# Performance work log

Measured on AMD Instinct MI355X. Metric: run time of the kernel, lower is better.

The kernel has to match this reference:

```python
import jax, jax.numpy as jnp
import numpy as np

E, T, D, H = 32, 65536, 512, 1024


def setup_inputs() -> dict:
    key = jax.random.key(0)
    k = jax.random.split(key, 7)
    norm = lambda kk, shp, sc: (jax.random.normal(kk, shp, jnp.float32) * sc)
    x = norm(k[0], (T, D), 1.0)
    w1 = norm(k[1], (E, D, H), D ** -0.5)   # per-expert up-proj (gate branch)
    b1 = norm(k[2], (E, H), 0.02)
    w3 = norm(k[3], (E, D, H), D ** -0.5)   # per-expert up-proj (linear branch)
    b3 = norm(k[4], (E, H), 0.02)
    w2 = norm(k[5], (E, H, D), H ** -0.5)   # per-expert down-proj
    b2 = norm(k[6], (E, D), 0.02)
    # tokens are pre-sorted by expert; uniform dispatch of T//E tokens per expert
    group_sizes = jnp.full((E,), T // E, jnp.int32)
    return dict(x=x, w1=w1, b1=b1, w3=w3, b3=b3, w2=w2, b2=b2,
                group_sizes=group_sizes)


def reference(x, w1, b1, w3, b3, w2, b2, group_sizes):
    # expert id per token, derived from contiguous group sizes
    bounds = jnp.cumsum(group_sizes)                       # [E]
    seg = jnp.searchsorted(bounds, jnp.arange(x.shape[0]), side='right')  # [T]
    # grouped GEMMs: per-expert weight bank applied to its contiguous token slab
    h1 = jax.lax.ragged_dot(x, w1, group_sizes) + b1[seg]  # [T,H]
    h3 = jax.lax.ragged_dot(x, w3, group_sizes) + b3[seg]  # [T,H]
    h = jax.nn.silu(h1) * h3                               # SwiGLU gate
    out = jax.lax.ragged_dot(h, w2, group_sizes) + b2[seg] # [T,D]
    return out
```

## Files before the change

### kernel.cpp

```cpp
#include <hip/hip_runtime.h>
#include <hip/hip_bf16.h>

#define TOK 65536
#define NE  32
#define DD  512
#define HH  1024
#define TPE 2048

typedef short s16x8  __attribute__((ext_vector_type(8)));
typedef float f32x16 __attribute__((ext_vector_type(16)));
using u16 = unsigned short;
using u32 = unsigned int;

__device__ __forceinline__ u16 f2bf(float f) {
  __bf16 h = (__bf16)f;
  return __builtin_bit_cast(u16, h);
}
__device__ __forceinline__ u32 pk2(float lo, float hi) {
  return (u32)f2bf(lo) | ((u32)f2bf(hi) << 16);
}
__device__ __forceinline__ int swz(int row, int colb) {
  return (row << 7) + (colb ^ ((row & 7) << 4));
}

#define MFMA(a, b, c) __builtin_amdgcn_mfma_f32_32x32x16_bf16(a, b, c, 0, 0, 0)
#define GLD(src, dst) __builtin_amdgcn_global_load_lds( \
    (const __attribute__((address_space(1))) void*)(src), \
    (__attribute__((address_space(3))) void*)(dst), 16, 0, 0)
#define SETP(n) __builtin_amdgcn_s_setprio(n)
#define SCHEDB() __builtin_amdgcn_sched_barrier(0)
#define SBAR()  __builtin_amdgcn_s_barrier()

__global__ __launch_bounds__(256) void p1_cvt_x(
    const float* __restrict__ x, u16* __restrict__ xb) {
  const size_t i = ((size_t)blockIdx.x * 256 + threadIdx.x) * 8;
  const float4 a = *(const float4*)(x + i);
  const float4 b = *(const float4*)(x + i + 4);
  uint4 v;
  v.x = pk2(a.x, a.y); v.y = pk2(a.z, a.w);
  v.z = pk2(b.x, b.y); v.w = pk2(b.z, b.w);
  *(uint4*)(xb + i) = v;
}

__global__ __launch_bounds__(256) void p2_w13t(
    const float* __restrict__ w1, const float* __restrict__ w3,
    u16* __restrict__ w13t) {
  __shared__ __align__(16) u16 L1[64 * 72], L3[64 * 72];
  const int bid = blockIdx.x;
  const int e = bid >> 7, rr = bid & 127;
  const int d0 = (rr & 7) << 6, h0 = (rr >> 3) << 6;
  const int t = threadIdx.x;
  const float* const s1 = w1 + (size_t)e * DD * HH + (size_t)d0 * HH + h0;
  const float* const s3 = w3 + (size_t)e * DD * HH + (size_t)d0 * HH + h0;
  const int cg = (t & 15) << 2, rbase = t >> 4;
#pragma unroll
  for (int j = 0; j < 4; ++j) {
    const int dr = rbase + (j << 4);
    const float4 a = *(const float4*)(s1 + (size_t)dr * HH + cg);
    const float4 b = *(const float4*)(s3 + (size_t)dr * HH + cg);
    L1[(cg + 0) * 72 + dr] = f2bf(a.x); L1[(cg + 1) * 72 + dr] = f2bf(a.y);
    L1[(cg + 2) * 72 + dr] = f2bf(a.z); L1[(cg + 3) * 72 + dr] = f2bf(a.w);
    L3[(cg + 0) * 72 + dr] = f2bf(b.x); L3[(cg + 1) * 72 + dr] = f2bf(b.y);
    L3[(cg + 2) * 72 + dr] = f2bf(b.z); L3[(cg + 3) * 72 + dr] = f2bf(b.w);
  }
  __syncthreads();
  u16* const dst = w13t + (size_t)e * (2 * HH) * DD;
  const int cb8 = (t & 7) << 3;
#pragma unroll
  for (int j = 0; j < 2; ++j) {
    const int nloc = (t >> 3) + (j << 5);
    const int n = h0 + nloc;
    const int R1 = ((n >> 5) << 6) + (n & 31);
    const uint4 v1 = *(const uint4*)(L1 + nloc * 72 + cb8);
    const uint4 v3 = *(const uint4*)(L3 + nloc * 72 + cb8);
    *(uint4*)(dst + (size_t)R1 * DD + d0 + cb8) = v1;
    *(uint4*)(dst + (size_t)(R1 + 32) * DD + d0 + cb8) = v3;
  }
}

__global__ __launch_bounds__(256) void p3_w2t(
    const float* __restrict__ w2, u16* __restrict__ w2t) {
  __shared__ __align__(16) u16 L[64 * 72];
  const int bid = blockIdx.x;
  const int e = bid >> 7, rr = bid & 127;
  const int d0 = (rr & 7) << 6, h0 = (rr >> 3) << 6;
  const int t = threadIdx.x;
  const float* const s = w2 + (size_t)e * HH * DD + (size_t)h0 * DD + d0;
  const int cg = (t & 15) << 2, rbase = t >> 4;
#pragma unroll
  for (int j = 0; j < 4; ++j) {
    const int hr = rbase + (j << 4);
    const float4 a = *(const float4*)(s + (size_t)hr * DD + cg);
    L[(cg + 0) * 72 + hr] = f2bf(a.x); L[(cg + 1) * 72 + hr] = f2bf(a.y);
    L[(cg + 2) * 72 + hr] = f2bf(a.z); L[(cg + 3) * 72 + hr] = f2bf(a.w);
  }
  __syncthreads();
  u16* const dst = w2t + (size_t)e * DD * HH;
  const int cb8 = (t & 7) << 3;
#pragma unroll
  for (int j = 0; j < 2; ++j) {
    const int dloc = (t >> 3) + (j << 5);
    const uint4 v = *(const uint4*)(L + dloc * 72 + cb8);
    *(uint4*)(dst + (size_t)(d0 + dloc) * HH + h0 + cb8) = v;
  }
}

template <int MODE>
__global__ __launch_bounds__(512, 2) void gemm4s(
    const u16* __restrict__ A, const u16* __restrict__ Bm,
    const float* __restrict__ bx, const float* __restrict__ by,
    void* __restrict__ outp) {
  constexpr int K  = MODE ? HH : DD;
  constexpr int NT = K >> 6;
  constexpr int NB = MODE ? 2 : 8;
  constexpr int NWG = NE * 8 * NB;
  __shared__ __align__(16) char lds[131072];

  int bid = blockIdx.x;
  bid = (bid & 7) * (NWG / 8) + (bid >> 3);
  const int e   = bid / (8 * NB);
  const int rr  = bid % (8 * NB);
  const int m_t = rr & 7;
  const int n_t = rr >> 3;
  const int rowbase = e * TPE + (m_t << 8);

  const int t = threadIdx.x;
  const int wv = t >> 6, lane = t & 63;
  const int l31 = lane & 31, half = lane >> 5;
  const int wm = wv >> 2, wn = wv & 3;

  const u16* const Abase = A + (size_t)rowbase * K;
  const u16* const Bbase = Bm + ((size_t)e * NB + n_t) * 256 * K;

  int srcoff0, srcoff1;
  {
    const int c0 = t,       lr0 = c0 >> 3, s0 = (c0 & 7) ^ (lr0 & 7);
    const int c1 = 512 + t, lr1 = c1 >> 3, s1 = (c1 & 7) ^ (lr1 & 7);
    srcoff0 = ((lr0 << 1) | (s0 >> 2)) * K + ((s0 & 3) << 3);
    srcoff1 = ((lr1 << 1) | (s1 >> 2)) * K + ((s1 & 3) << 3);
  }
  const int t16 = t << 4;

  auto stageQ = [&](int tau, int q) {
    const u16* const src = ((q & 1) ? Bbase : Abase) + tau * 64 + (q >> 1) * 32;
    char* const dst = lds + ((tau & 1) << 16) + (q << 14);
    GLD(src + srcoff0, dst + t16);
    GLD(src + srcoff1, dst + 8192 + t16);
  };

  const int lrow_off = l31 >> 1;
  const int pbit = l31 & 1;
  const int sw7 = lrow_off & 7;
  const int sA0 = (((pbit << 2) | 0 | half) ^ sw7) << 4;
  const int sA1 = (((pbit << 2) | 2 | half) ^ sw7) << 4;
  const int aoff = ((wm << 6) + lrow_off) << 7;
  const int boff = ((wn << 5) + lrow_off) << 7;

  f32x16 acc[4][2] = {};
  s16x8 b00{}, b01{}, b10{}, b11{};

#define VM4 asm volatile("s_waitcnt vmcnt(4)" ::: "memory")
#define VM0 asm volatile("s_waitcnt vmcnt(0)" ::: "memory")
#define LGKM0 asm volatile("s_waitcnt lgkmcnt(0)" ::: "memory")
#define NOPV ((void)0)

#define PHASE(CB, KH, MH, DOB, STG, VM) do { \
  const char* const Aq = (CB) + ((KH) << 15); \
  const char* const Bq = Aq + 16384; \
  if (DOB) { \
    b00 = *(const s16x8*)(Bq + boff + 0 * 2048 + sA0); \
    b01 = *(const s16x8*)(Bq + boff + 1 * 2048 + sA0); \
    b10 = *(const s16x8*)(Bq + boff + 0 * 2048 + sA1); \
    b11 = *(const s16x8*)(Bq + boff + 1 * 2048 + sA1); \
  } \
  const s16x8 a0 = *(const s16x8*)(Aq + aoff + (2 * (MH)) * 2048 + sA0); \
  const s16x8 a1 = *(const s16x8*)(Aq + aoff + (2 * (MH)) * 2048 + sA1); \
  const s16x8 a2 = *(const s16x8*)(Aq + aoff + (2 * (MH) + 1) * 2048 + sA0); \
  const s16x8 a3 = *(const s16x8*)(Aq + aoff + (2 * (MH) + 1) * 2048 + sA1); \
  STG; VM; \
  SCHEDB(); SBAR(); LGKM0; SCHEDB(); \
  SETP(1); \
  acc[2 * (MH)][0]     = MFMA(a0, b00, acc[2 * (MH)][0]); \
  acc[2 * (MH)][1]     = MFMA(a0, b01, acc[2 * (MH)][1]); \
  acc[2 * (MH)][0]     = MFMA(a1, b10, acc[2 * (MH)][0]); \
  acc[2 * (MH)][1]     = MFMA(a1, b11, acc[2 * (MH)][1]); \
  acc[2 * (MH) + 1][0] = MFMA(a2, b00, acc[2 * (MH) + 1][0]); \
  acc[2 * (MH) + 1][1] = MFMA(a2, b01, acc[2 * (MH) + 1][1]); \
  acc[2 * (MH) + 1][0] = MFMA(a3, b10, acc[2 * (MH) + 1][0]); \
  acc[2 * (MH) + 1][1] = MFMA(a3, b11, acc[2 * (MH) + 1][1]); \
  SETP(0); \
} while (0)

  stageQ(0, 0); stageQ(0, 1); stageQ(0, 2); stageQ(0, 3);
  VM4; SCHEDB(); SBAR();

  for (int kt = 0; kt < NT - 1; ++kt) {
    const char* const cb = lds + ((kt & 1) << 16);
    PHASE(cb, 0, 0, true,  (stageQ(kt + 1, 0), stageQ(kt + 1, 1)), NOPV);
    PHASE(cb, 0, 1, false, NOPV, VM4);
    PHASE(cb, 1, 0, true,  (stageQ(kt + 1, 2), stageQ(kt + 1, 3)), NOPV);
    PHASE(cb, 1, 1, false, NOPV, VM4);
  }
  {
    const char* const cb = lds + (((NT - 1) & 1) << 16);
    PHASE(cb, 0, 0, true,  NOPV, NOPV);
    PHASE(cb, 0, 1, false, NOPV, VM0);
    PHASE(cb, 1, 0, true,  NOPV, NOPV);
    PHASE(cb, 1, 1, false, NOPV, NOPV);
  }

#undef PHASE
#undef VM4
#undef VM0
#undef LGKM0
#undef NOPV

  if constexpr (MODE == 0) {
    const int g = (n_t << 2) + wn;
    const int hcol = (g << 5) + l31;
    const float bv1 = bx[e * HH + hcol];
    const float bv3 = by[e * HH + hcol];
    u16* const hp = (u16*)outp;
#pragma unroll
    for (int mf = 0; mf < 4; ++mf) {
#pragma unroll
      for (int rg = 0; rg < 16; ++rg) {
        const int grow = rowbase + (wm << 7) + (mf << 5) +
                         (rg & 3) + ((rg >> 2) << 3) + (half << 2);
        const float s1 = acc[mf][0][rg] + bv1;
        const float s3 = acc[mf][1][rg] + bv3;
        hp[(size_t)grow * HH + hcol] = f2bf(s1 * s3 / (1.0f + __expf(-s1)));
      }
    }
  } else {
    float* const op = (float*)outp;
#pragma unroll
    for (int mf = 0; mf < 4; ++mf) {
#pragma unroll
      for (int nf = 0; nf < 2; ++nf) {
        const int col = (n_t << 8) + (wn << 6) + (nf << 5) + l31;
        const float bv = bx[e * DD + col];
#pragma unroll
        for (int rg = 0; rg < 16; ++rg) {
          const int grow = rowbase + (wm << 7) + (mf << 5) +
                           (rg & 3) + ((rg >> 2) << 3) + (half << 2);
          op[(size_t)grow * DD + col] = acc[mf][nf][rg] + bv;
        }
      }
    }
  }
}

__global__ __launch_bounds__(256, 2) void k1_up_swiglu(
    const float* __restrict__ x,  const float* __restrict__ w1,
    const float* __restrict__ b1, const float* __restrict__ w3,
    const float* __restrict__ b3, u16* __restrict__ hbuf) {
  __shared__ __align__(16) char lds[32768];
  char* const As  = lds;
  char* const B1s = lds + 16384;
  char* const B3s = lds + 24576;
  const int bid = blockIdx.x;
  const int e = bid >> 8, rr = bid & 255;
  const int m_t = rr & 15, n_t = rr >> 4;
  const int rowbase = e * TPE + (m_t << 7), colbase = n_t << 6;
  const int t = threadIdx.x, wv = t >> 6, lane = t & 63;
  const int l31 = lane & 31, half = lane >> 5;
  const int wm = wv >> 1, wn = wv & 1;
  const int ag = t & 15, am0 = t >> 4, bn = t & 63, bk0 = t >> 6;
  const float* const xb = x + (size_t)rowbase * DD + (ag << 2);
  const size_t woff = (size_t)e * (DD * HH) + colbase + bn;
  const float* const w1b = w1 + woff;
  const float* const w3b = w3 + woff;
  float4 ra[8]; float rb1[16], rb3[16];
  auto gload = [&](int kt) {
    const float* xp = xb + (kt << 6);
#pragma unroll
    for (int j = 0; j < 8; ++j)
      ra[j] = *(const float4*)(xp + (size_t)(am0 + (j << 4)) * DD);
#pragma unroll
    for (int j = 0; j < 2; ++j) {
      const int k0 = (kt << 6) + ((bk0 + (j << 2)) << 3);
#pragma unroll
      for (int i = 0; i < 8; ++i) {
        rb1[(j << 3) + i] = w1b[(size_t)(k0 + i) * HH];
        rb3[(j << 3) + i] = w3b[(size_t)(k0 + i) * HH];
      }
    }
  };
  f32x16 acc10 = {}, acc11 = {}, acc30 = {}, acc31 = {};
  gload(0);
  for (int kt = 0; kt < 8; ++kt) {
    if (kt) __syncthreads();
#pragma unroll
    for (int j = 0; j < 8; ++j) {
      const int m = am0 + (j << 4);
      uint2 v; v.x = pk2(ra[j].x, ra[j].y); v.y = pk2(ra[j].z, ra[j].w);
      *(uint2*)(As + swz(m, ag << 3)) = v;
    }
#pragma unroll
    for (int j = 0; j < 2; ++j) {
      const int kg = bk0 + (j << 2);
      uint4 v;
      v.x = pk2(rb1[(j << 3) + 0], rb1[(j << 3) + 1]);
      v.y = pk2(rb1[(j << 3) + 2], rb1[(j << 3) + 3]);
      v.z = pk2(rb1[(j << 3) + 4], rb1[(j << 3) + 5]);
      v.w = pk2(rb1[(j << 3) + 6], rb1[(j << 3) + 7]);
      *(uint4*)(B1s + swz(bn, kg << 4)) = v;
      v.x = pk2(rb3[(j << 3) + 0], rb3[(j << 3) + 1]);
      v.y = pk2(rb3[(j << 3) + 2], rb3[(j << 3) + 3]);
      v.z = pk2(rb3[(j << 3) + 4], rb3[(j << 3) + 5]);
      v.w = pk2(rb3[(j << 3) + 6], rb3[(j << 3) + 7]);
      *(uint4*)(B3s + swz(bn, kg << 4)) = v;
    }
    __syncthreads();
    if (kt < 7) gload(kt + 1);
#pragma unroll
    for (int kk = 0; kk < 4; ++kk) {
      const int colb = (kk << 5) + (half << 4);
      const s16x8 a0 = *(const s16x8*)(As  + swz((wm << 6) + l31,      colb));
      const s16x8 a1 = *(const s16x8*)(As  + swz((wm << 6) + 32 + l31, colb));
      const s16x8 f1 = *(const s16x8*)(B1s + swz((wn << 5) + l31,      colb));
      const s16x8 f3 = *(const s16x8*)(B3s + swz((wn << 5) + l31,      colb));
      acc10 = MFMA(a0, f1, acc10); acc30 = MFMA(a0, f3, acc30);
      acc11 = MFMA(a1, f1, acc11); acc31 = MFMA(a1, f3, acc31);
    }
  }
  const int gcol = colbase + (wn << 5) + l31;
  const float bv1 = b1[e * HH + gcol], bv3 = b3[e * HH + gcol];
  u16* const hp = hbuf + gcol;
#pragma unroll
  for (int mb = 0; mb < 2; ++mb) {
    const f32x16 A1 = mb ? acc11 : acc10;
    const f32x16 A3 = mb ? acc31 : acc30;
#pragma unroll
    for (int rg = 0; rg < 16; ++rg) {
      const int grow = rowbase + (wm << 6) + (mb << 5) +
                       (rg & 3) + ((rg >> 2) << 3) + (half << 2);
      const float s1 = A1[rg] + bv1, s3 = A3[rg] + bv3;
      hp[(size_t)grow * HH] = f2bf(s1 * s3 / (1.0f + __expf(-s1)));
    }
  }
}

__global__ __launch_bounds__(256, 2) void k2_down(
    const u16* __restrict__ hbuf, const float* __restrict__ w2,
    const float* __restrict__ b2, float* __restrict__ out) {
  __shared__ __align__(16) char lds[32768];
  char* const As = lds;
  char* const Bs = lds + 16384;
  const int bid = blockIdx.x;
  const int e = bid >> 6, rr = bid & 63;
  const int m_t = rr & 15, n_t = rr >> 4;
  const int rowbase = e * TPE + (m_t << 7), colbase = n_t << 7;
  const int t = threadIdx.x, wv = t >> 6, lane = t & 63;
  const int l31 = lane & 31, half = lane >> 5;
  const int wm = wv >> 1, wn = wv & 1;
  const int ag = t & 7, am0 = t >> 3, bnn = t & 127, bk0 = t >> 7;
  const u16* const hb = hbuf + (size_t)rowbase * HH + (ag << 3);
  const float* const w2b = w2 + (size_t)e * (HH * DD) + colbase + bnn;
  uint4 ra[4]; float rb[32];
  auto gload = [&](int kt) {
#pragma unroll
    for (int j = 0; j < 4; ++j)
      ra[j] = *(const uint4*)(hb + (size_t)(am0 + (j << 5)) * HH + (kt << 6));
#pragma unroll
    for (int j = 0; j < 4; ++j) {
      const int k0 = (kt << 6) + ((bk0 + (j << 1)) << 3);
#pragma unroll
      for (int i = 0; i < 8; ++i)
        rb[(j << 3) + i] = w2b[(size_t)(k0 + i) * DD];
    }
  };
  f32x16 c00 = {}, c01 = {}, c10 = {}, c11 = {};
  gload(0);
  for (int kt = 0; kt < 16; ++kt) {
    if (kt) __syncthreads();
#pragma unroll
    for (int j = 0; j < 4; ++j)
      *(uint4*)(As + swz(am0 + (j << 5), ag << 4)) = ra[j];
#pragma unroll
    for (int j = 0; j < 4; ++j) {
      const int kg = bk0 + (j << 1);
      uint4 v;
      v.x = pk2(rb[(j << 3) + 0], rb[(j << 3) + 1]);
      v.y = pk2(rb[(j << 3) + 2], rb[(j << 3) + 3]);
      v.z = pk2(rb[(j << 3) + 4], rb[(j << 3) + 5]);
      v.w = pk2(rb[(j << 3) + 6], rb[(j << 3) + 7]);
      *(uint4*)(Bs + swz(bnn, kg << 4)) = v;
    }
    __syncthreads();
    if (kt < 15) gload(kt + 1);
#pragma unroll
    for (int kk = 0; kk < 4; ++kk) {
      const int colb = (kk << 5) + (half << 4);
      const s16x8 af0 = *(const s16x8*)(As + swz((wm << 6) + l31,      colb));
      const s16x8 af1 = *(const s16x8*)(As + swz((wm << 6) + 32 + l31, colb));
      const s16x8 bf0 = *(const s16x8*)(Bs + swz((wn << 6) + l31,      colb));
      const s16x8 bf1 = *(const s16x8*)(Bs + swz((wn << 6) + 32 + l31, colb));
      c00 = MFMA(af0, bf0, c00); c01 = MFMA(af0, bf1, c01);
      c10 = MFMA(af1, bf0, c10); c11 = MFMA(af1, bf1, c11);
    }
  }
#pragma unroll
  for (int mb = 0; mb < 2; ++mb) {
#pragma unroll
    for (int nb = 0; nb < 2; ++nb) {
      const f32x16 c = mb ? (nb ? c11 : c10) : (nb ? c01 : c00);
      const int gcol = colbase + (wn << 6) + (nb << 5) + l31;
      const float bv = b2[e * DD + gcol];
#pragma unroll
      for (int rg = 0; rg < 16; ++rg) {
        const int grow = rowbase + (wm << 6) + (mb << 5) +
                         (rg & 3) + ((rg >> 2) << 3) + (half << 2);
        out[(size_t)grow * DD + gcol] = c[rg] + bv;
      }
    }
  }
}

extern "C" void kernel_launch(void* const* d_in, const int* in_sizes, int n_in,
                              void* d_out, int out_size, void* d_ws, size_t ws_size,
                              hipStream_t stream) {
  const float* x  = (const float*)d_in[0];
  const float* w1 = (const float*)d_in[1];
  const float* b1 = (const float*)d_in[2];
  const float* w3 = (const float*)d_in[3];
  const float* b3 = (const float*)d_in[4];
  const float* w2 = (const float*)d_in[5];
  const float* b2 = (const float*)d_in[6];

  const size_t W13T_B = (size_t)NE * 2 * HH * DD * 2;
  const size_t W2T_B  = (size_t)NE * DD * HH * 2;
  const size_t H_B    = (size_t)TOK * HH * 2;

  if (ws_size >= W13T_B + W2T_B + H_B) {
    u16* const xb   = (u16*)d_out;
    u16* const w13t = (u16*)d_ws;
    u16* const w2t  = (u16*)((char*)d_ws + W13T_B);
    u16* const hbuf = (u16*)((char*)d_ws + W13T_B + W2T_B);

    p1_cvt_x<<<dim3(TOK * DD / 2048), dim3(256), 0, stream>>>(x, xb);
    p2_w13t <<<dim3(NE * 128),        dim3(256), 0, stream>>>(w1, w3, w13t);
    p3_w2t  <<<dim3(NE * 128),        dim3(256), 0, stream>>>(w2, w2t);
    gemm4s<0><<<dim3(NE * 64), dim3(512), 0, stream>>>(xb, w13t, b1, b3, hbuf);
    gemm4s<1><<<dim3(NE * 16), dim3(512), 0, stream>>>(hbuf, w2t, b2, nullptr, d_out);
  } else {
    u16* hbuf = (ws_size >= H_B) ? (u16*)d_ws : (u16*)d_out;
    k1_up_swiglu<<<dim3(NE * 256), dim3(256), 0, stream>>>(x, w1, b1, w3, b3, hbuf);
    k2_down<<<dim3(NE * 64), dim3(256), 0, stream>>>(hbuf, w2, b2, (float*)d_out);
  }
}
```

Before: 366.3 us.

## Replace up-projection mega-tile GEMM with smaller single-buffered 128x128 tile kernel

```diff
diff --git a/kernel.cpp b/kernel.cpp
--- a/kernel.cpp
+++ b/kernel.cpp
@@ -105,14 +105,91 @@
   }
 }
 
-template <int MODE>
-__global__ __launch_bounds__(512, 2) void gemm4s(
+__global__ __launch_bounds__(256, 3) void g0_up(
     const u16* __restrict__ A, const u16* __restrict__ Bm,
     const float* __restrict__ bx, const float* __restrict__ by,
-    void* __restrict__ outp) {
-  constexpr int K  = MODE ? HH : DD;
+    u16* __restrict__ hp) {
+  constexpr int K = DD;
+  __shared__ __align__(16) char lds[32768];
+  char* const As = lds;
+  char* const Bs = lds + 16384;
+
+  int bid = blockIdx.x;
+  bid = (bid & 7) * (NE * 256 / 8) + (bid >> 3);
+  const int e   = bid >> 8;
+  const int rr  = bid & 255;
+  const int m_t = rr & 15;
+  const int n_t = rr >> 4;
+  const int rowbase = e * TPE + (m_t << 7);
+
+  const int t = threadIdx.x, wv = t >> 6, lane = t & 63;
+  const int l31 = lane & 31, half = lane >> 5;
+  const int wm = wv >> 1, wn = wv & 1;
+
+  const u16* const Abase = A + (size_t)rowbase * K;
+  const u16* const Bbase = Bm + ((size_t)e * 2048 + (size_t)n_t * 128) * K;
+
+  int soff[4], lb[4];
+#pragma unroll
+  for (int j = 0; j < 4; ++j) {
+    const int idx = (j << 8) + t;
+    const int r = idx >> 3;
+    const int cb = ((idx & 7) << 4) ^ ((r & 7) << 4);
+    soff[j] = r * K + (cb >> 1);
+    lb[j] = ((j << 8) + (wv << 6)) << 4;
+  }
+
+  f32x16 c00 = {}, c01 = {}, c10 = {}, c11 = {};
+  const int sw  = (l31 & 7) << 4;
+  const int ra0 = ((wm << 6) + l31) << 7, ra1 = ra0 + (32 << 7);
+  const int rb0 = ((wn << 6) + l31) << 7, rb1 = rb0 + (32 << 7);
+
+  for (int kt = 0; kt < 8; ++kt) {
+    const u16* const Ak = Abase + (kt << 6);
+    const u16* const Bk = Bbase + (kt << 6);
+#pragma unroll
+    for (int j = 0; j < 4; ++j) {
+      GLD(Ak + soff[j], As + lb[j]);
+      GLD(Bk + soff[j], Bs + lb[j]);
+    }
+    __syncthreads();
+#pragma unroll
+    for (int ks = 0; ks < 4; ++ks) {
+      const int ko = ((ks << 5) + (half << 4)) ^ sw;
+      const s16x8 a0 = *(const s16x8*)(As + ra0 + ko);
+      const s16x8 a1 = *(const s16x8*)(As + ra1 + ko);
+      const s16x8 b0 = *(const s16x8*)(Bs + rb0 + ko);
+      const s16x8 b1 = *(const s16x8*)(Bs + rb1 + ko);
+      c00 = MFMA(a0, b0, c00); c01 = MFMA(a0, b1, c01);
+      c10 = MFMA(a1, b0, c10); c11 = MFMA(a1, b1, c11);
+    }
+    __syncthreads();
+  }
+
+  const int hcol = (n_t << 6) + (wn << 5) + l31;
+  const float bv1 = bx[e * HH + hcol];
+  const float bv3 = by[e * HH + hcol];
+#pragma unroll
+  for (int mf = 0; mf < 2; ++mf) {
+    const f32x16 A1 = mf ? c10 : c00;
+    const f32x16 A3 = mf ? c11 : c01;
+#pragma unroll
+    for (int rg = 0; rg < 16; ++rg) {
+      const int grow = rowbase + (wm << 6) + (mf << 5) +
+                       (rg & 3) + ((rg >> 2) << 3) + (half << 2);
+      const float s1 = A1[rg] + bv1;
+      const float s3 = A3[rg] + bv3;
+      hp[(size_t)grow * HH + hcol] = f2bf(s1 * s3 / (1.0f + __expf(-s1)));
+    }
+  }
+}
+
+__global__ __launch_bounds__(512, 2) void g1_down(
+    const u16* __restrict__ A, const u16* __restrict__ Bm,
+    const float* __restrict__ bx, float* __restrict__ op) {
+  constexpr int K  = HH;
   constexpr int NT = K >> 6;
-  constexpr int NB = MODE ? 2 : 8;
+  constexpr int NB = 2;
   constexpr int NWG = NE * 8 * NB;
   __shared__ __align__(16) char lds[131072];
 
@@ -215,37 +292,17 @@
 #undef LGKM0
 #undef NOPV
 
-  if constexpr (MODE == 0) {
-    const int g = (n_t << 2) + wn;
-    const int hcol = (g << 5) + l31;
-    const float bv1 = bx[e * HH + hcol];
-    const float bv3 = by[e * HH + hcol];
-    u16* const hp = (u16*)outp;
-#pragma unroll
-    for (int mf = 0; mf < 4; ++mf) {
+#pragma unroll
+  for (int mf = 0; mf < 4; ++mf) {
+#pragma unroll
+    for (int nf = 0; nf < 2; ++nf) {
+      const int col = (n_t << 8) + (wn << 6) + (nf << 5) + l31;
+      const float bv = bx[e * DD + col];
 #pragma unroll
       for (int rg = 0; rg < 16; ++rg) {
         const int grow = rowbase + (wm << 7) + (mf << 5) +
                          (rg & 3) + ((rg >> 2) << 3) + (half << 2);
-        const float s1 = acc[mf][0][rg] + bv1;
-        const float s3 = acc[mf][1][rg] + bv3;
-        hp[(size_t)grow * HH + hcol] = f2bf(s1 * s3 / (1.0f + __expf(-s1)));
-      }
-    }
-  } else {
-    float* const op = (float*)outp;
-#pragma unroll
-    for (int mf = 0; mf < 4; ++mf) {
-#pragma unroll
-      for (int nf = 0; nf < 2; ++nf) {
-        const int col = (n_t << 8) + (wn << 6) + (nf << 5) + l31;
-        const float bv = bx[e * DD + col];
-#pragma unroll
-        for (int rg = 0; rg < 16; ++rg) {
-          const int grow = rowbase + (wm << 7) + (mf << 5) +
-                           (rg & 3) + ((rg >> 2) << 3) + (half << 2);
-          op[(size_t)grow * DD + col] = acc[mf][nf][rg] + bv;
-        }
+        op[(size_t)grow * DD + col] = acc[mf][nf][rg] + bv;
       }
     }
   }
@@ -442,8 +499,8 @@
     p1_cvt_x<<<dim3(TOK * DD / 2048), dim3(256), 0, stream>>>(x, xb);
     p2_w13t <<<dim3(NE * 128),        dim3(256), 0, stream>>>(w1, w3, w13t);
     p3_w2t  <<<dim3(NE * 128),        dim3(256), 0, stream>>>(w2, w2t);
-    gemm4s<0><<<dim3(NE * 64), dim3(512), 0, stream>>>(xb, w13t, b1, b3, hbuf);
-    gemm4s<1><<<dim3(NE * 16), dim3(512), 0, stream>>>(hbuf, w2t, b2, nullptr, d_out);
+    g0_up  <<<dim3(NE * 256), dim3(256), 0, stream>>>(xb, w13t, b1, b3, hbuf);
+    g1_down<<<dim3(NE * 16),  dim3(512), 0, stream>>>(hbuf, w2t, b2, (float*)d_out);
   } else {
     u16* hbuf = (ws_size >= H_B) ? (u16*)d_ws : (u16*)d_out;
     k1_up_swiglu<<<dim3(NE * 256), dim3(256), 0, stream>>>(x, w1, b1, w3, b3, hbuf);
```

After: 354.8 us. 1.03x faster.

## Merge prep kernels into one launch and make up-projection GEMM persistent per expert

Applied to the files above, without the earlier changes.

```diff
diff --git a/kernel.cpp b/kernel.cpp
--- a/kernel.cpp
+++ b/kernel.cpp
@@ -31,88 +31,218 @@
 #define SCHEDB() __builtin_amdgcn_sched_barrier(0)
 #define SBAR()  __builtin_amdgcn_s_barrier()
 
-__global__ __launch_bounds__(256) void p1_cvt_x(
-    const float* __restrict__ x, u16* __restrict__ xb) {
-  const size_t i = ((size_t)blockIdx.x * 256 + threadIdx.x) * 8;
-  const float4 a = *(const float4*)(x + i);
-  const float4 b = *(const float4*)(x + i + 4);
-  uint4 v;
-  v.x = pk2(a.x, a.y); v.y = pk2(a.z, a.w);
-  v.z = pk2(b.x, b.y); v.w = pk2(b.z, b.w);
-  *(uint4*)(xb + i) = v;
-}
-
-__global__ __launch_bounds__(256) void p2_w13t(
-    const float* __restrict__ w1, const float* __restrict__ w3,
-    u16* __restrict__ w13t) {
+__global__ __launch_bounds__(256) void p123(
+    const float* __restrict__ x,  const float* __restrict__ w1,
+    const float* __restrict__ w3, const float* __restrict__ w2,
+    u16* __restrict__ xb, u16* __restrict__ w13t, u16* __restrict__ w2t) {
   __shared__ __align__(16) u16 L1[64 * 72], L3[64 * 72];
-  const int bid = blockIdx.x;
-  const int e = bid >> 7, rr = bid & 127;
-  const int d0 = (rr & 7) << 6, h0 = (rr >> 3) << 6;
+  const int bid0 = blockIdx.x;
   const int t = threadIdx.x;
-  const float* const s1 = w1 + (size_t)e * DD * HH + (size_t)d0 * HH + h0;
-  const float* const s3 = w3 + (size_t)e * DD * HH + (size_t)d0 * HH + h0;
+
+  if (bid0 < 16384) {
+    const size_t i = ((size_t)bid0 * 256 + t) * 8;
+    const float4 a = *(const float4*)(x + i);
+    const float4 b = *(const float4*)(x + i + 4);
+    uint4 v;
+    v.x = pk2(a.x, a.y); v.y = pk2(a.z, a.w);
+    v.z = pk2(b.x, b.y); v.w = pk2(b.z, b.w);
+    *(uint4*)(xb + i) = v;
+    return;
+  }
   const int cg = (t & 15) << 2, rbase = t >> 4;
-#pragma unroll
-  for (int j = 0; j < 4; ++j) {
-    const int dr = rbase + (j << 4);
-    const float4 a = *(const float4*)(s1 + (size_t)dr * HH + cg);
-    const float4 b = *(const float4*)(s3 + (size_t)dr * HH + cg);
-    L1[(cg + 0) * 72 + dr] = f2bf(a.x); L1[(cg + 1) * 72 + dr] = f2bf(a.y);
-    L1[(cg + 2) * 72 + dr] = f2bf(a.z); L1[(cg + 3) * 72 + dr] = f2bf(a.w);
-    L3[(cg + 0) * 72 + dr] = f2bf(b.x); L3[(cg + 1) * 72 + dr] = f2bf(b.y);
-    L3[(cg + 2) * 72 + dr] = f2bf(b.z); L3[(cg + 3) * 72 + dr] = f2bf(b.w);
-  }
-  __syncthreads();
-  u16* const dst = w13t + (size_t)e * (2 * HH) * DD;
   const int cb8 = (t & 7) << 3;
-#pragma unroll
-  for (int j = 0; j < 2; ++j) {
-    const int nloc = (t >> 3) + (j << 5);
-    const int n = h0 + nloc;
-    const int R1 = ((n >> 5) << 6) + (n & 31);
-    const uint4 v1 = *(const uint4*)(L1 + nloc * 72 + cb8);
-    const uint4 v3 = *(const uint4*)(L3 + nloc * 72 + cb8);
-    *(uint4*)(dst + (size_t)R1 * DD + d0 + cb8) = v1;
-    *(uint4*)(dst + (size_t)(R1 + 32) * DD + d0 + cb8) = v3;
-  }
-}
-
-__global__ __launch_bounds__(256) void p3_w2t(
-    const float* __restrict__ w2, u16* __restrict__ w2t) {
-  __shared__ __align__(16) u16 L[64 * 72];
-  const int bid = blockIdx.x;
-  const int e = bid >> 7, rr = bid & 127;
-  const int d0 = (rr & 7) << 6, h0 = (rr >> 3) << 6;
-  const int t = threadIdx.x;
-  const float* const s = w2 + (size_t)e * HH * DD + (size_t)h0 * DD + d0;
-  const int cg = (t & 15) << 2, rbase = t >> 4;
-#pragma unroll
-  for (int j = 0; j < 4; ++j) {
-    const int hr = rbase + (j << 4);
-    const float4 a = *(const float4*)(s + (size_t)hr * DD + cg);
-    L[(cg + 0) * 72 + hr] = f2bf(a.x); L[(cg + 1) * 72 + hr] = f2bf(a.y);
-    L[(cg + 2) * 72 + hr] = f2bf(a.z); L[(cg + 3) * 72 + hr] = f2bf(a.w);
-  }
-  __syncthreads();
-  u16* const dst = w2t + (size_t)e * DD * HH;
-  const int cb8 = (t & 7) << 3;
-#pragma unroll
-  for (int j = 0; j < 2; ++j) {
-    const int dloc = (t >> 3) + (j << 5);
-    const uint4 v = *(const uint4*)(L + dloc * 72 + cb8);
-    *(uint4*)(dst + (size_t)(d0 + dloc) * HH + h0 + cb8) = v;
-  }
-}
-
-template <int MODE>
-__global__ __launch_bounds__(512, 2) void gemm4s(
+  if (bid0 < 16384 + NE * 128) {
+    const int bid = bid0 - 16384;
+    const int e = bid >> 7, rr = bid & 127;
+    const int d0 = (rr & 7) << 6, h0 = (rr >> 3) << 6;
+    const float* const s1 = w1 + (size_t)e * DD * HH + (size_t)d0 * HH + h0;
+    const float* const s3 = w3 + (size_t)e * DD * HH + (size_t)d0 * HH + h0;
+#pragma unroll
+    for (int j = 0; j < 4; ++j) {
+      const int dr = rbase + (j << 4);
+      const float4 a = *(const float4*)(s1 + (size_t)dr * HH + cg);
+      const float4 b = *(const float4*)(s3 + (size_t)dr * HH + cg);
+      L1[(cg + 0) * 72 + dr] = f2bf(a.x); L1[(cg + 1) * 72 + dr] = f2bf(a.y);
+      L1[(cg + 2) * 72 + dr] = f2bf(a.z); L1[(cg + 3) * 72 + dr] = f2bf(a.w);
+      L3[(cg + 0) * 72 + dr] = f2bf(b.x); L3[(cg + 1) * 72 + dr] = f2bf(b.y);
+      L3[(cg + 2) * 72 + dr] = f2bf(b.z); L3[(cg + 3) * 72 + dr] = f2bf(b.w);
+    }
+    __syncthreads();
+    u16* const dst = w13t + (size_t)e * (2 * HH) * DD;
+#pragma unroll
+    for (int j = 0; j < 2; ++j) {
+      const int nloc = (t >> 3) + (j << 5);
+      const int n = h0 + nloc;
+      const int R1 = ((n >> 5) << 6) + (n & 31);
+      const uint4 v1 = *(const uint4*)(L1 + nloc * 72 + cb8);
+      const uint4 v3 = *(const uint4*)(L3 + nloc * 72 + cb8);
+      *(uint4*)(dst + (size_t)R1 * DD + d0 + cb8) = v1;
+      *(uint4*)(dst + (size_t)(R1 + 32) * DD + d0 + cb8) = v3;
+    }
+  } else {
+    const int bid = bid0 - 16384 - NE * 128;
+    const int e = bid >> 7, rr = bid & 127;
+    const int d0 = (rr & 7) << 6, h0 = (rr >> 3) << 6;
+    const float* const s = w2 + (size_t)e * HH * DD + (size_t)h0 * DD + d0;
+#pragma unroll
+    for (int j = 0; j < 4; ++j) {
+      const int hr = rbase + (j << 4);
+      const float4 a = *(const float4*)(s + (size_t)hr * DD + cg);
+      L1[(cg + 0) * 72 + hr] = f2bf(a.x); L1[(cg + 1) * 72 + hr] = f2bf(a.y);
+      L1[(cg + 2) * 72 + hr] = f2bf(a.z); L1[(cg + 3) * 72 + hr] = f2bf(a.w);
+    }
+    __syncthreads();
+    u16* const dst = w2t + (size_t)e * DD * HH;
+#pragma unroll
+    for (int j = 0; j < 2; ++j) {
+      const int dloc = (t >> 3) + (j << 5);
+      const uint4 v = *(const uint4*)(L1 + dloc * 72 + cb8);
+      *(uint4*)(dst + (size_t)(d0 + dloc) * HH + h0 + cb8) = v;
+    }
+  }
+}
+
+__global__ __launch_bounds__(512, 2) void g0_pers(
     const u16* __restrict__ A, const u16* __restrict__ Bm,
     const float* __restrict__ bx, const float* __restrict__ by,
-    void* __restrict__ outp) {
-  constexpr int K  = MODE ? HH : DD;
+    u16* __restrict__ hp) {
+  constexpr int K   = DD;
+  constexpr int NVT = 64;
+  __shared__ __align__(16) char lds[131072];
+
+  int bid = blockIdx.x;
+  bid = (bid & 7) * 32 + (bid >> 3);
+  const int e   = bid >> 3;
+  const int n_t = bid & 7;
+
+  const int t = threadIdx.x;
+  const int wv = t >> 6, lane = t & 63;
+  const int l31 = lane & 31, half = lane >> 5;
+  const int wm = wv >> 2, wn = wv & 3;
+
+  const u16* const Abase = A + (size_t)e * TPE * K;
+  const u16* const Bbase = Bm + ((size_t)e * 8 + n_t) * 256 * K;
+
+  int srcoff0, srcoff1;
+  {
+    const int c0 = t,       lr0 = c0 >> 3, s0 = (c0 & 7) ^ (lr0 & 7);
+    const int c1 = 512 + t, lr1 = c1 >> 3, s1 = (c1 & 7) ^ (lr1 & 7);
+    srcoff0 = ((lr0 << 1) | (s0 >> 2)) * K + ((s0 & 3) << 3);
+    srcoff1 = ((lr1 << 1) | (s1 >> 2)) * K + ((s1 & 3) << 3);
+  }
+  const int t16 = t << 4;
+
+  auto stageQ = [&](int vt1, int q) {
+    const int mi = vt1 >> 3, kt = vt1 & 7;
+    const u16* const src =
+        ((q & 1) ? Bbase : (Abase + ((size_t)mi << 8) * K)) +
+        kt * 64 + (q >> 1) * 32;
+    char* const dst = lds + ((vt1 & 1) << 16) + (q << 14);
+    GLD(src + srcoff0, dst + t16);
+    GLD(src + srcoff1, dst + 8192 + t16);
+  };
+
+  const int lrow_off = l31 >> 1;
+  const int pbit = l31 & 1;
+  const int sw7 = lrow_off & 7;
+  const int sA0 = (((pbit << 2) | 0 | half) ^ sw7) << 4;
+  const int sA1 = (((pbit << 2) | 2 | half) ^ sw7) << 4;
+  const int aoff = ((wm << 6) + lrow_off) << 7;
+  const int boff = ((wn << 5) + lrow_off) << 7;
+
+  const int g = (n_t << 2) + wn;
+  const int hcol = (g << 5) + l31;
+  const float bv1 = bx[e * HH + hcol];
+  const float bv3 = by[e * HH + hcol];
+
+  f32x16 acc[4][2] = {};
+  s16x8 b00{}, b01{}, b10{}, b11{};
+
+#define VM4 asm volatile("s_waitcnt vmcnt(4)" ::: "memory")
+#define VM0 asm volatile("s_waitcnt vmcnt(0)" ::: "memory")
+#define NOPV ((void)0)
+
+#define PHASE(CB, KH, MH, DOB, STG, VM) do { \
+  const char* const Aq = (CB) + ((KH) << 15); \
+  const char* const Bq = Aq + 16384; \
+  if (DOB) { \
+    b00 = *(const s16x8*)(Bq + boff + 0 * 2048 + sA0); \
+    b01 = *(const s16x8*)(Bq + boff + 1 * 2048 + sA0); \
+    b10 = *(const s16x8*)(Bq + boff + 0 * 2048 + sA1); \
+    b11 = *(const s16x8*)(Bq + boff + 1 * 2048 + sA1); \
+  } \
+  const s16x8 a0 = *(const s16x8*)(Aq + aoff + (2 * (MH)) * 2048 + sA0); \
+  const s16x8 a1 = *(const s16x8*)(Aq + aoff + (2 * (MH)) * 2048 + sA1); \
+  const s16x8 a2 = *(const s16x8*)(Aq + aoff + (2 * (MH) + 1) * 2048 + sA0); \
+  const s16x8 a3 = *(const s16x8*)(Aq + aoff + (2 * (MH) + 1) * 2048 + sA1); \
+  STG; VM; \
+  SCHEDB(); SBAR(); \
+  asm volatile("s_waitcnt lgkmcnt(0)" ::: "memory"); \
+  SCHEDB(); \
+  SETP(1); \
+  acc[2 * (MH)][0]     = MFMA(a0, b00, acc[2 * (MH)][0]); \
+  acc[2 * (MH)][1]     = MFMA(a0, b01, acc[2 * (MH)][1]); \
+  acc[2 * (MH)][0]     = MFMA(a1, b10, acc[2 * (MH)][0]); \
+  acc[2 * (MH)][1]     = MFMA(a1, b11, acc[2 * (MH)][1]); \
+  acc[2 * (MH) + 1][0] = MFMA(a2, b00, acc[2 * (MH) + 1][0]); \
+  acc[2 * (MH) + 1][1] = MFMA(a2, b01, acc[2 * (MH) + 1][1]); \
+  acc[2 * (MH) + 1][0] = MFMA(a3, b10, acc[2 * (MH) + 1][0]); \
+  acc[2 * (MH) + 1][1] = MFMA(a3, b11, acc[2 * (MH) + 1][1]); \
+  SETP(0); \
+} while (0)
+
+  auto epilogue = [&](int mi) {
+    const int rowbase = e * TPE + (mi << 8);
+#pragma unroll
+    for (int mf = 0; mf < 4; ++mf) {
+#pragma unroll
+      for (int rg = 0; rg < 16; ++rg) {
+        const int grow = rowbase + (wm << 7) + (mf << 5) +
+                         (rg & 3) + ((rg >> 2) << 3) + (half << 2);
+        const float s1 = acc[mf][0][rg] + bv1;
+        const float s3 = acc[mf][1][rg] + bv3;
+        hp[(size_t)grow * HH + hcol] = f2bf(s1 * s3 / (1.0f + __expf(-s1)));
+      }
+    }
+#pragma unroll
+    for (int mf = 0; mf < 4; ++mf) {
+      acc[mf][0] = (f32x16){};
+      acc[mf][1] = (f32x16){};
+    }
+  };
+
+  stageQ(0, 0); stageQ(0, 1); stageQ(0, 2); stageQ(0, 3);
+  VM4; SCHEDB(); SBAR();
+
+  for (int vt = 0; vt < NVT - 1; ++vt) {
+    const char* const cb = lds + ((vt & 1) << 16);
+    PHASE(cb, 0, 0, true,  (stageQ(vt + 1, 0), stageQ(vt + 1, 1)), NOPV);
+    PHASE(cb, 0, 1, false, NOPV, VM4);
+    PHASE(cb, 1, 0, true,  (stageQ(vt + 1, 2), stageQ(vt + 1, 3)), NOPV);
+    PHASE(cb, 1, 1, false, NOPV, VM4);
+    if ((vt & 7) == 7) epilogue(vt >> 3);
+  }
+  {
+    const char* const cb = lds + (((NVT - 1) & 1) << 16);
+    PHASE(cb, 0, 0, true,  NOPV, NOPV);
+    PHASE(cb, 0, 1, false, NOPV, VM0);
+    PHASE(cb, 1, 0, true,  NOPV, NOPV);
+    PHASE(cb, 1, 1, false, NOPV, NOPV);
+  }
+  epilogue(7);
+
+#undef PHASE
+#undef VM4
+#undef VM0
+#undef NOPV
+}
+
+__global__ __launch_bounds__(512, 2) void g1_down(
+    const u16* __restrict__ A, const u16* __restrict__ Bm,
+    const float* __restrict__ bx, float* __restrict__ op) {
+  constexpr int K  = HH;
   constexpr int NT = K >> 6;
-  constexpr int NB = MODE ? 2 : 8;
+  constexpr int NB = 2;
   constexpr int NWG = NE * 8 * NB;
   __shared__ __align__(16) char lds[131072];
 
@@ -215,37 +345,17 @@
 #undef LGKM0
 #undef NOPV
 
-  if constexpr (MODE == 0) {
-    const int g = (n_t << 2) + wn;
-    const int hcol = (g << 5) + l31;
-    const float bv1 = bx[e * HH + hcol];
-    const float bv3 = by[e * HH + hcol];
-    u16* const hp = (u16*)outp;
-#pragma unroll
-    for (int mf = 0; mf < 4; ++mf) {
+#pragma unroll
+  for (int mf = 0; mf < 4; ++mf) {
+#pragma unroll
+    for (int nf = 0; nf < 2; ++nf) {
+      const int col = (n_t << 8) + (wn << 6) + (nf << 5) + l31;
+      const float bv = bx[e * DD + col];
 #pragma unroll
       for (int rg = 0; rg < 16; ++rg) {
         const int grow = rowbase + (wm << 7) + (mf << 5) +
                          (rg & 3) + ((rg >> 2) << 3) + (half << 2);
-        const float s1 = acc[mf][0][rg] + bv1;
-        const float s3 = acc[mf][1][rg] + bv3;
-        hp[(size_t)grow * HH + hcol] = f2bf(s1 * s3 / (1.0f + __expf(-s1)));
-      }
-    }
-  } else {
-    float* const op = (float*)outp;
-#pragma unroll
-    for (int mf = 0; mf < 4; ++mf) {
-#pragma unroll
-      for (int nf = 0; nf < 2; ++nf) {
-        const int col = (n_t << 8) + (wn << 6) + (nf << 5) + l31;
-        const float bv = bx[e * DD + col];
-#pragma unroll
-        for (int rg = 0; rg < 16; ++rg) {
-          const int grow = rowbase + (wm << 7) + (mf << 5) +
-                           (rg & 3) + ((rg >> 2) << 3) + (half << 2);
-          op[(size_t)grow * DD + col] = acc[mf][nf][rg] + bv;
-        }
+        op[(size_t)grow * DD + col] = acc[mf][nf][rg] + bv;
       }
     }
   }
@@ -439,11 +549,10 @@
     u16* const w2t  = (u16*)((char*)d_ws + W13T_B);
     u16* const hbuf = (u16*)((char*)d_ws + W13T_B + W2T_B);
 
-    p1_cvt_x<<<dim3(TOK * DD / 2048), dim3(256), 0, stream>>>(x, xb);
-    p2_w13t <<<dim3(NE * 128),        dim3(256), 0, stream>>>(w1, w3, w13t);
-    p3_w2t  <<<dim3(NE * 128),        dim3(256), 0, stream>>>(w2, w2t);
-    gemm4s<0><<<dim3(NE * 64), dim3(512), 0, stream>>>(xb, w13t, b1, b3, hbuf);
-    gemm4s<1><<<dim3(NE * 16), dim3(512), 0, stream>>>(hbuf, w2t, b2, nullptr, d_out);
+    p123   <<<dim3(16384 + NE * 256), dim3(256), 0, stream>>>(
+        x, w1, w3, w2, xb, w13t, w2t);
+    g0_pers<<<dim3(256), dim3(512), 0, stream>>>(xb, w13t, b1, b3, hbuf);
+    g1_down<<<dim3(NE * 16), dim3(512), 0, stream>>>(hbuf, w2t, b2, (float*)d_out);
   } else {
     u16* hbuf = (ws_size >= H_B) ? (u16*)d_ws : (u16*)d_out;
     k1_up_swiglu<<<dim3(NE * 256), dim3(256), 0, stream>>>(x, w1, b1, w3, b3, hbuf);
```

Measured after the change: 360.9 us. No clear change (-1.5%).
